# Kernel optimization log

Measured on AMD Instinct MI355X. Metric: run time of the kernel, lower is better.

The kernel has to match this reference:

```python
import jax, jax.numpy as jnp
import numpy as np

N_ATOMS = 10000
N_EDGES = 160000
C_EMB = 32          # embedding_size
N_RBF = 32          # radial_features
Z_MAX = 119
CUTOFF = 5.0


def setup_inputs() -> dict:
    key = jax.random.key(0)
    ks = jax.random.split(key, 8)
    atomic_numbers = jax.random.randint(ks[0], (N_ATOMS,), 0, Z_MAX)
    neighbour_index = jax.random.randint(ks[1], (2, N_EDGES), 0, N_ATOMS)
    edge_vectors = jax.random.normal(ks[2], (N_EDGES, 3), dtype=jnp.float32) * 2.0
    z_table = jax.random.normal(ks[3], (Z_MAX, C_EMB), dtype=jnp.float32) * 0.1
    z_map_W = jax.random.normal(ks[4], (C_EMB, 2 * C_EMB), dtype=jnp.float32) * 0.1
    dense_W = jax.random.normal(ks[5], (3 * C_EMB, N_RBF), dtype=jnp.float32) * 0.1
    dense_b = jax.random.normal(ks[6], (3 * C_EMB,), dtype=jnp.float32) * 0.1
    # PhysNet-style exponential RBF parameters (graph-pes ExponentialRBF)
    c_inf = float(np.exp(-CUTOFF))
    rbf_centres = jnp.linspace(c_inf, 1.0, N_RBF, dtype=jnp.float32)
    beta_val = (2.0 / N_RBF * (1.0 - c_inf)) ** -2
    rbf_beta = jnp.full((N_RBF,), beta_val, dtype=jnp.float32)
    return {
        'atomic_numbers': atomic_numbers,
        'neighbour_index': neighbour_index,
        'edge_vectors': edge_vectors,
        'z_table': z_table,
        'z_map_W': z_map_W,
        'dense_W': dense_W,
        'dense_b': dense_b,
        'rbf_beta': rbf_beta,
        'rbf_centres': rbf_centres,
    }


def reference(atomic_numbers, neighbour_index, edge_vectors, z_table,
              z_map_W, dense_W, dense_b, rbf_beta, rbf_centres):
    # --- geometry -----------------------------------------------------
    r = jnp.linalg.norm(edge_vectors, axis=-1)              # [E]
    r_hat = edge_vectors / r[:, None]                       # [E,3]
    vx, vy, vz = r_hat[:, 0], r_hat[:, 1], r_hat[:, 2]
    zero = jnp.zeros_like(vx)
    # skew-symmetric A_0 (matches torch stack ordering)
    A0 = jnp.stack([zero, -vz, vy,
                    vz, zero, -vx,
                    -vy, vx, zero], axis=1).reshape(-1, 3, 3)   # [E,3,3]
    eye = jnp.eye(3, dtype=edge_vectors.dtype)
    outer = r_hat[:, :, None] * r_hat[:, None, :]            # [E,3,3]
    trace_mean = jnp.trace(outer, axis1=-2, axis2=-1) / 3.0  # [E]
    S0 = 0.5 * (outer + jnp.swapaxes(outer, -1, -2)) - trace_mean[:, None, None] * eye
    # --- species embedding ---------------------------------------------
    h_atom = z_table[atomic_numbers]                         # [N,C]
    h_i = h_atom[neighbour_index[0]]                         # [E,C]
    h_j = h_atom[neighbour_index[1]]                         # [E,C]
    h_z = jnp.concatenate([h_i, h_j], axis=-1) @ z_map_W.T   # [E,C]
    # --- radial embedding (exp RBF -> Linear, x cosine envelope) -------
    rbf = jnp.exp(-rbf_beta[None, :] *
                  (jnp.exp(-r)[:, None] - rbf_centres[None, :]) ** 2)  # [E,R]
    h_r = rbf @ dense_W.T + dense_b                          # [E,3C]
    env = jnp.where(r < CUTOFF,
                    0.5 * (jnp.cos(jnp.pi * r / CUTOFF) + 1.0), 0.0)
    h_r = h_r * env[:, None]
    # --- combine --------------------------------------------------------
    c = h_r * jnp.tile(h_z, (1, 3))                          # [E,3C]
    C = h_z.shape[-1]
    c_I, c_A, c_S = c[:, :C], c[:, C:2 * C], c[:, 2 * C:]
    X_I = c_I[:, :, None, None] * eye                        # [E,C,3,3]
    X_A = c_A[:, :, None, None] * A0[:, None, :, :]          # [E,C,3,3]
    X_S = c_S[:, :, None, None] * S0[:, None, :, :]          # [E,C,3,3]
    return X_I, X_A, X_S
```

## Files before the change

### kernel.cpp

```cpp
#include <hip/hip_runtime.h>

#define N_EDGES 160000
#define C_EMB 32
#define N_RBF 32
#define Z_MAX 119

typedef float floatx4 __attribute__((ext_vector_type(4)));

#define PI_F 3.14159265358979323f
#define RSZ ((size_t)N_EDGES * 288)

__global__ __launch_bounds__(256) void k0_tables(
    const float* __restrict__ zt,
    const float* __restrict__ zw,
    float* __restrict__ FG)
{
    int i = blockIdx.x * 256 + threadIdx.x;
    if (i >= 2 * Z_MAX * C_EMB) return;
    int which = i / (Z_MAX * C_EMB);
    int j = i - which * Z_MAX * C_EMB;
    int z = j >> 5, cc = j & 31;
    const float* wrow = zw + cc * 64 + which * 32;
    const float* zrow = zt + z * 32;
    float acc = 0.0f;
    #pragma unroll
    for (int k = 0; k < 32; ++k) acc += zrow[k] * wrow[k];
    FG[i] = acc;
}

#define EPA 64
#define TA 256

__global__ __launch_bounds__(TA) void kA_features(
    const int* __restrict__ atomic_numbers,
    const int* __restrict__ nbr,
    const float* __restrict__ ev,
    const float* __restrict__ dense_W,
    const float* __restrict__ dense_b,
    const float* __restrict__ rbf_beta,
    const float* __restrict__ rbf_centres,
    const float* __restrict__ FG,
    float* __restrict__ rec)
{
    __shared__ int   s_zi[EPA];
    __shared__ int   s_zj[EPA];
    __shared__ float s_rbf[EPA][N_RBF];
    __shared__ float s_env[EPA];

    const int tid = threadIdx.x;
    const int e0 = blockIdx.x * EPA;

    if (tid < EPA)            s_zi[tid]       = atomic_numbers[nbr[e0 + tid]];
    else if (tid < 2 * EPA)   s_zj[tid - EPA] = atomic_numbers[nbr[N_EDGES + e0 + tid - EPA]];

    for (int idx = tid; idx < EPA * N_RBF; idx += TA) {
        int e = idx >> 5, n = idx & 31, ge = e0 + e;
        float x = ev[ge * 3 + 0], y = ev[ge * 3 + 1], z = ev[ge * 3 + 2];
        float r = sqrtf(x * x + y * y + z * z);
        float d = __expf(-r) - rbf_centres[n];
        s_rbf[e][n] = __expf(-rbf_beta[n] * d * d);
        if (n == 0)
            s_env[e] = (r < 5.0f) ? 0.5f * (__cosf(PI_F * r * 0.2f) + 1.0f) : 0.0f;
    }

    for (int idx = tid; idx < EPA * 27; idx += TA) {
        int e = idx / 27, t = idx - e * 27, ge = e0 + e;
        float x = ev[ge * 3 + 0], y = ev[ge * 3 + 1], z = ev[ge * 3 + 2];
        float rinv = rsqrtf(x * x + y * y + z * z);
        float vx = x * rinv, vy = y * rinv, vz = z * rinv;
        float val;
        if (t < 9) {
            val = (t == 0 || t == 4 || t == 8) ? 1.0f : 0.0f;
        } else if (t < 18) {
            int p = t - 9;
            switch (p) {
                case 1: val = -vz; break;
                case 2: val =  vy; break;
                case 3: val =  vz; break;
                case 5: val = -vx; break;
                case 6: val = -vy; break;
                case 7: val =  vx; break;
                default: val = 0.0f; break;
            }
        } else {
            int p = t - 18;
            int i = p / 3, j = p - 3 * i;
            float ri = (i == 0) ? vx : ((i == 1) ? vy : vz);
            float rj = (j == 0) ? vx : ((j == 1) ? vy : vz);
            val = ri * rj - ((i == j) ? (1.0f / 3.0f) : 0.0f);
        }
        rec[(size_t)ge * 128 + 96 + t] = val;
    }
    __syncthreads();

    const float* Ft = FG;
    const float* Gt = FG + Z_MAX * C_EMB;
    for (int idx = tid; idx < EPA * 96; idx += TA) {
        int e = idx / 96, m = idx - e * 96, ge = e0 + e;
        int cc = m & 31;
        const float4* Wd  = (const float4*)(dense_W + m * 32);
        const float4* rb4 = (const float4*)s_rbf[e];
        float acc = dense_b[m];
        #pragma unroll
        for (int n = 0; n < 8; ++n) {
            float4 w = Wd[n]; float4 rv = rb4[n];
            acc += w.x * rv.x + w.y * rv.y + w.z * rv.z + w.w * rv.w;
        }
        float hz = Ft[s_zi[e] * 32 + cc] + Gt[s_zj[e] * 32 + cc];
        rec[(size_t)ge * 128 + m] = acc * s_env[e] * hz;
    }
}

#define BBLK 1024
#define BT 256
#define NPAIR (N_EDGES / 2)

__global__ __launch_bounds__(BT) void kB_expand(
    const float* __restrict__ rec,
    float* __restrict__ out)
{
    __shared__ float lds[BT / 64][256];

    const int tid  = threadIdx.x;
    const int lane = tid & 63;
    const int w    = tid >> 6;
    const int gw   = blockIdx.x * (BT / 64) + w;
    const int NW   = BBLK * (BT / 64);

    int el[3], ccc[3][4], ppp[3][4];
    #pragma unroll
    for (int s = 0; s < 3; ++s) {
        int q = s * 64 + lane;
        int e_l = q / 72;
        int qq = q - 72 * e_l;
        el[s] = (q < 144) ? e_l : 0;
        #pragma unroll
        for (int u = 0; u < 4; ++u) {
            int f = 4 * qq + u;
            ccc[s][u] = f / 9;
            ppp[s][u] = f - 9 * (f / 9);
        }
    }

    float* sc = lds[w];
    const floatx4* rec4 = (const floatx4*)rec;
    const int half = lane >> 5, sub = lane & 31;

    floatx4 g = rec4[(size_t)(2 * gw + half) * 32 + sub];

    for (int p = gw; p < NPAIR; p += NW) {
        ((floatx4*)sc)[half * 32 + sub] = g;

        int pn = p + NW;
        floatx4 gn = g;
        if (pn < NPAIR) gn = rec4[(size_t)(2 * pn + half) * 32 + sub];

        #pragma unroll
        for (int r = 0; r < 3; ++r) {
            float* ob = out + (size_t)r * RSZ + (size_t)(2 * p) * 288;
            #pragma unroll
            for (int s = 0; s < 2; ++s) {
                floatx4 v;
                #pragma unroll
                for (int u = 0; u < 4; ++u) {
                    v[u] = sc[el[s] * 128 + 32 * r + ccc[s][u]]
                         * sc[el[s] * 128 + 96 + 9 * r + ppp[s][u]];
                }
                ((floatx4*)ob)[s * 64 + lane] = v;
            }
            if (lane < 16) {
                floatx4 v;
                #pragma unroll
                for (int u = 0; u < 4; ++u) {
                    v[u] = sc[el[2] * 128 + 32 * r + ccc[2][u]]
                         * sc[el[2] * 128 + 96 + 9 * r + ppp[2][u]];
                }
                ((floatx4*)ob)[128 + lane] = v;
            }
        }
        g = gn;
    }
}

#define EPBF 16
#define TF 256

__global__ __launch_bounds__(TF) void edge_embed_fallback(
    const int* __restrict__ atomic_numbers,
    const int* __restrict__ nbr,
    const float* __restrict__ ev,
    const float* __restrict__ z_table,
    const float* __restrict__ z_map_W,
    const float* __restrict__ dense_W,
    const float* __restrict__ dense_b,
    const float* __restrict__ rbf_beta,
    const float* __restrict__ rbf_centres,
    float* __restrict__ out)
{
    __shared__ float s_hi[EPBF][C_EMB];
    __shared__ float s_hj[EPBF][C_EMB];
    __shared__ float s_rbf[EPBF][N_RBF];
    __shared__ float s_hz[EPBF][C_EMB];
    __shared__ float s_c[EPBF][96];
    __shared__ float s_basis[EPBF][28];

    const int tid = threadIdx.x;
    const int e0 = blockIdx.x * EPBF;

    for (int idx = tid; idx < EPBF * C_EMB; idx += TF) {
        int e = idx >> 5, k = idx & 31, ge = e0 + e;
        s_hi[e][k] = z_table[atomic_numbers[nbr[ge]] * C_EMB + k];
        s_hj[e][k] = z_table[atomic_numbers[nbr[N_EDGES + ge]] * C_EMB + k];
    }
    for (int idx = tid; idx < EPBF * N_RBF; idx += TF) {
        int e = idx >> 5, n = idx & 31, ge = e0 + e;
        float x = ev[ge * 3 + 0], y = ev[ge * 3 + 1], z = ev[ge * 3 + 2];
        float r = sqrtf(x * x + y * y + z * z);
        float d = __expf(-r) - rbf_centres[n];
        s_rbf[e][n] = __expf(-rbf_beta[n] * d * d);
        if (n == 0)
            s_basis[e][27] = (r < 5.0f) ? 0.5f * (__cosf(PI_F * r * 0.2f) + 1.0f) : 0.0f;
    }
    for (int idx = tid; idx < EPBF * 27; idx += TF) {
        int e = idx / 27, t = idx - e * 27, ge = e0 + e;
        float x = ev[ge * 3 + 0], y = ev[ge * 3 + 1], z = ev[ge * 3 + 2];
        float rinv = rsqrtf(x * x + y * y + z * z);
        float vx = x * rinv, vy = y * rinv, vz = z * rinv;
        float val;
        if (t < 9) val = (t == 0 || t == 4 || t == 8) ? 1.0f : 0.0f;
        else if (t < 18) {
            int p = t - 9;
            switch (p) {
                case 1: val = -vz; break;
                case 2: val =  vy; break;
                case 3: val =  vz; break;
                case 5: val = -vx; break;
                case 6: val = -vy; break;
                case 7: val =  vx; break;
                default: val = 0.0f; break;
            }
        } else {
            int p = t - 18;
            int i = p / 3, j = p - 3 * i;
            float ri = (i == 0) ? vx : ((i == 1) ? vy : vz);
            float rj = (j == 0) ? vx : ((j == 1) ? vy : vz);
            val = ri * rj - ((i == j) ? (1.0f / 3.0f) : 0.0f);
        }
        s_basis[e][t] = val;
    }
    __syncthreads();
    for (int idx = tid; idx < EPBF * C_EMB; idx += TF) {
        int e = idx >> 5, cc = idx & 31;
        const float4* Wi  = (const float4*)(z_map_W + cc * 64);
        const float4* hi4 = (const float4*)s_hi[e];
        const float4* hj4 = (const float4*)s_hj[e];
        float acc = 0.0f;
        #pragma unroll
        for (int k = 0; k < 8; ++k) {
            float4 w = Wi[k]; float4 h = hi4[k];
            acc += w.x * h.x + w.y * h.y + w.z * h.z + w.w * h.w;
        }
        #pragma unroll
        for (int k = 0; k < 8; ++k) {
            float4 w = Wi[8 + k]; float4 h = hj4[k];
            acc += w.x * h.x + w.y * h.y + w.z * h.z + w.w * h.w;
        }
        s_hz[e][cc] = acc;
    }
    __syncthreads();
    for (int idx = tid; idx < EPBF * 96; idx += TF) {
        int e = idx / 96, m = idx - e * 96;
        int cc = m & 31;
        const float4* Wd  = (const float4*)(dense_W + m * 32);
        const float4* rb4 = (const float4*)s_rbf[e];
        float acc = dense_b[m];
        #pragma unroll
        for (int n = 0; n < 8; ++n) {
            float4 w = Wd[n]; float4 rv = rb4[n];
            acc += w.x * rv.x + w.y * rv.y + w.z * rv.z + w.w * rv.w;
        }
        s_c[e][m] = acc * s_basis[e][27] * s_hz[e][cc];
    }
    __syncthreads();
    float* outI = out + (size_t)e0 * 288;
    float* outA = out + RSZ + (size_t)e0 * 288;
    float* outS = out + 2 * RSZ + (size_t)e0 * 288;
    const int NQ = EPBF * 288 / 4;
    for (int q = tid; q < NQ; q += TF) {
        int fbase = q * 4;
        floatx4 aI, aA, aS;
        #pragma unroll
        for (int u = 0; u < 4; ++u) {
            int f = fbase + u;
            int e = f / 288;
            int rem = f - e * 288;
            int cc = rem / 9;
            int p = rem - cc * 9;
            aI[u] = s_c[e][cc]      * s_basis[e][p];
            aA[u] = s_c[e][32 + cc] * s_basis[e][9 + p];
            aS[u] = s_c[e][64 + cc] * s_basis[e][18 + p];
        }
        ((floatx4*)outI)[q] = aI;
        ((floatx4*)outA)[q] = aA;
        ((floatx4*)outS)[q] = aS;
    }
}

extern "C" void kernel_launch(void* const* d_in, const int* in_sizes, int n_in,
                              void* d_out, int out_size, void* d_ws, size_t ws_size,
                              hipStream_t stream) {
    const int*   an  = (const int*)d_in[0];
    const int*   nbr = (const int*)d_in[1];
    const float* ev  = (const float*)d_in[2];
    const float* zt  = (const float*)d_in[3];
    const float* zw  = (const float*)d_in[4];
    const float* dw  = (const float*)d_in[5];
    const float* db  = (const float*)d_in[6];
    const float* rb  = (const float*)d_in[7];
    const float* rc  = (const float*)d_in[8];
    float* outp = (float*)d_out;

    const size_t rec_f = (size_t)N_EDGES * 128;
    const size_t fg_f  = 2 * Z_MAX * C_EMB;
    const size_t need  = (rec_f + fg_f) * sizeof(float);

    if (ws_size >= need) {
        float* rec = (float*)d_ws;
        float* FG  = rec + rec_f;
        k0_tables<<<dim3((2 * Z_MAX * C_EMB + 255) / 256), 256, 0, stream>>>(zt, zw, FG);
        kA_features<<<dim3(N_EDGES / EPA), TA, 0, stream>>>(
            an, nbr, ev, dw, db, rb, rc, FG, rec);
        kB_expand<<<dim3(BBLK), BT, 0, stream>>>(rec, outp);
    } else {
        edge_embed_fallback<<<dim3(N_EDGES / EPBF), TF, 0, stream>>>(
            an, nbr, ev, zt, zw, dw, db, rb, rc, outp);
    }
}
```

Baseline: 378.0 us.

## Expand one edge per wavefront with direct global loads instead of LDS staging

The expand kernel now gives each wavefront one edge per iteration instead of a pair staged through shared memory. Each lane reads its coefficient and basis values straight from the per-edge record, which should hit in cache, and picks between two adjacent channel values with a select. It drops the LDS round trip and the software prefetch, and doubles the grid to 2048 blocks. The trade-off is more scalar global loads per lane and more underused lanes on the 72-vector tail (only 8 of 64 lanes active).

Result: slower. 468.9 us (+24.1%).

```diff
diff --git a/kernel.cpp b/kernel.cpp
--- a/kernel.cpp
+++ b/kernel.cpp
@@ -111,74 +111,76 @@
     }
 }
 
-#define BBLK 1024
-#define BT 256
-#define NPAIR (N_EDGES / 2)
-
-__global__ __launch_bounds__(BT) void kB_expand(
+#define TB 256
+#define NB 2048
+
+__global__ __launch_bounds__(TB) void kB_expand(
     const float* __restrict__ rec,
     float* __restrict__ out)
 {
-    __shared__ float lds[BT / 64][256];
-
-    const int tid  = threadIdx.x;
-    const int lane = tid & 63;
-    const int w    = tid >> 6;
-    const int gw   = blockIdx.x * (BT / 64) + w;
-    const int NW   = BBLK * (BT / 64);
-
-    int el[3], ccc[3][4], ppp[3][4];
+    const int lane = threadIdx.x & 63;
+    const int gw   = (blockIdx.x * TB + threadIdx.x) >> 6;
+    const int NW   = NB * (TB >> 6);
+
+    int cbase[2];
+    int sel[2][4];
+    int pp[2][4];
     #pragma unroll
-    for (int s = 0; s < 3; ++s) {
+    for (int s = 0; s < 2; ++s) {
         int q = s * 64 + lane;
-        int e_l = q / 72;
-        int qq = q - 72 * e_l;
-        el[s] = (q < 144) ? e_l : 0;
+        if (q >= 72) q = 71;
+        int f0 = 4 * q;
+        cbase[s] = f0 / 9;
         #pragma unroll
         for (int u = 0; u < 4; ++u) {
-            int f = 4 * qq + u;
-            ccc[s][u] = f / 9;
-            ppp[s][u] = f - 9 * (f / 9);
-        }
-    }
-
-    float* sc = lds[w];
-    const floatx4* rec4 = (const floatx4*)rec;
-    const int half = lane >> 5, sub = lane & 31;
-
-    floatx4 g = rec4[(size_t)(2 * gw + half) * 32 + sub];
-
-    for (int p = gw; p < NPAIR; p += NW) {
-        ((floatx4*)sc)[half * 32 + sub] = g;
-
-        int pn = p + NW;
-        floatx4 gn = g;
-        if (pn < NPAIR) gn = rec4[(size_t)(2 * pn + half) * 32 + sub];
-
+            int f = f0 + u;
+            int c = f / 9;
+            sel[s][u] = c - cbase[s];
+            pp[s][u]  = f - 9 * c;
+        }
+    }
+    const bool t1 = (lane < 8);
+
+    for (int e = gw; e < N_EDGES; e += NW) {
+        const float* row = rec + (size_t)e * 128;
+
+        float c0a[3], c0b[3], b0[3][4];
         #pragma unroll
         for (int r = 0; r < 3; ++r) {
-            float* ob = out + (size_t)r * RSZ + (size_t)(2 * p) * 288;
+            c0a[r] = row[32 * r + cbase[0]];
+            c0b[r] = row[32 * r + cbase[0] + 1];
             #pragma unroll
-            for (int s = 0; s < 2; ++s) {
-                floatx4 v;
+            for (int u = 0; u < 4; ++u)
+                b0[r][u] = row[96 + 9 * r + pp[0][u]];
+        }
+        float c1a[3], c1b[3], b1[3][4];
+        if (t1) {
+            #pragma unroll
+            for (int r = 0; r < 3; ++r) {
+                c1a[r] = row[32 * r + cbase[1]];
+                c1b[r] = row[32 * r + cbase[1] + 1];
                 #pragma unroll
-                for (int u = 0; u < 4; ++u) {
-                    v[u] = sc[el[s] * 128 + 32 * r + ccc[s][u]]
-                         * sc[el[s] * 128 + 96 + 9 * r + ppp[s][u]];
-                }
-                ((floatx4*)ob)[s * 64 + lane] = v;
+                for (int u = 0; u < 4; ++u)
+                    b1[r][u] = row[96 + 9 * r + pp[1][u]];
             }
-            if (lane < 16) {
-                floatx4 v;
+        }
+
+        #pragma unroll
+        for (int r = 0; r < 3; ++r) {
+            float* ob = out + (size_t)r * RSZ + (size_t)e * 288;
+            floatx4 v;
+            #pragma unroll
+            for (int u = 0; u < 4; ++u)
+                v[u] = (sel[0][u] ? c0b[r] : c0a[r]) * b0[r][u];
+            *(floatx4*)(ob + 4 * lane) = v;
+            if (t1) {
+                floatx4 w;
                 #pragma unroll
-                for (int u = 0; u < 4; ++u) {
-                    v[u] = sc[el[2] * 128 + 32 * r + ccc[2][u]]
-                         * sc[el[2] * 128 + 96 + 9 * r + ppp[2][u]];
-                }
-                ((floatx4*)ob)[128 + lane] = v;
+                for (int u = 0; u < 4; ++u)
+                    w[u] = (sel[1][u] ? c1b[r] : c1a[r]) * b1[r][u];
+                *(floatx4*)(ob + 256 + 4 * lane) = w;
             }
         }
-        g = gn;
     }
 }
 
@@ -330,7 +332,7 @@
         k0_tables<<<dim3((2 * Z_MAX * C_EMB + 255) / 256), 256, 0, stream>>>(zt, zw, FG);
         kA_features<<<dim3(N_EDGES / EPA), TA, 0, stream>>>(
             an, nbr, ev, dw, db, rb, rc, FG, rec);
-        kB_expand<<<dim3(BBLK), BT, 0, stream>>>(rec, outp);
+        kB_expand<<<dim3(NB), TB, 0, stream>>>(rec, outp);
     } else {
         edge_embed_fallback<<<dim3(N_EDGES / EPBF), TF, 0, stream>>>(
             an, nbr, ev, zt, zw, dw, db, rb, rc, outp);
```

## Replace persistent wave expand kernel with per-block streaming kernel and hoist geometry

Applied to the files above, without the earlier changes.

The output-expansion kernel goes from a persistent grid, where each wave loops over edge pairs with a register prefetch, to a non-persistent grid of 10000 blocks. Each block stages 16 edges of the compact record into shared memory and writes all three output tensors with float4 stores. The features kernel now computes r, exp(-r), the envelope and the unit vector once per edge into shared memory, so the RBF and tensor loops no longer recompute them. The trade-offs are more block launches, the loss of cross-iteration prefetch, and per-element index divisions in the store loop.

Result: faster. 360.9 us (-4.5%).

```diff
diff --git a/kernel.cpp b/kernel.cpp
--- a/kernel.cpp
+++ b/kernel.cpp
@@ -18,7 +18,7 @@
     int i = blockIdx.x * 256 + threadIdx.x;
     if (i >= 2 * Z_MAX * C_EMB) return;
     int which = i / (Z_MAX * C_EMB);
-    int j = i - which * Z_MAX * C_EMB;
+    int j = i - which * (Z_MAX * C_EMB);
     int z = j >> 5, cc = j & 31;
     const float* wrow = zw + cc * 64 + which * 32;
     const float* zrow = zt + z * 32;
@@ -42,32 +42,38 @@
     const float* __restrict__ FG,
     float* __restrict__ rec)
 {
-    __shared__ int   s_zi[EPA];
-    __shared__ int   s_zj[EPA];
+    __shared__ float s_er[EPA], s_env[EPA];
+    __shared__ float s_vx[EPA], s_vy[EPA], s_vz[EPA];
+    __shared__ int   s_zi[EPA], s_zj[EPA];
     __shared__ float s_rbf[EPA][N_RBF];
-    __shared__ float s_env[EPA];
 
     const int tid = threadIdx.x;
     const int e0 = blockIdx.x * EPA;
 
-    if (tid < EPA)            s_zi[tid]       = atomic_numbers[nbr[e0 + tid]];
-    else if (tid < 2 * EPA)   s_zj[tid - EPA] = atomic_numbers[nbr[N_EDGES + e0 + tid - EPA]];
+    if (tid < EPA) {
+        int ge = e0 + tid;
+        float x = ev[ge * 3 + 0], y = ev[ge * 3 + 1], z = ev[ge * 3 + 2];
+        float r2 = x * x + y * y + z * z;
+        float r = sqrtf(r2);
+        float rinv = rsqrtf(r2);
+        s_er[tid]  = __expf(-r);
+        s_env[tid] = (r < 5.0f) ? 0.5f * (__cosf(PI_F * r * 0.2f) + 1.0f) : 0.0f;
+        s_vx[tid] = x * rinv; s_vy[tid] = y * rinv; s_vz[tid] = z * rinv;
+    } else if (tid < 2 * EPA) {
+        s_zi[tid - EPA] = atomic_numbers[nbr[e0 + tid - EPA]];
+    } else if (tid < 3 * EPA) {
+        s_zj[tid - 2 * EPA] = atomic_numbers[nbr[N_EDGES + e0 + tid - 2 * EPA]];
+    }
+    __syncthreads();
 
     for (int idx = tid; idx < EPA * N_RBF; idx += TA) {
-        int e = idx >> 5, n = idx & 31, ge = e0 + e;
-        float x = ev[ge * 3 + 0], y = ev[ge * 3 + 1], z = ev[ge * 3 + 2];
-        float r = sqrtf(x * x + y * y + z * z);
-        float d = __expf(-r) - rbf_centres[n];
+        int e = idx >> 5, n = idx & 31;
+        float d = s_er[e] - rbf_centres[n];
         s_rbf[e][n] = __expf(-rbf_beta[n] * d * d);
-        if (n == 0)
-            s_env[e] = (r < 5.0f) ? 0.5f * (__cosf(PI_F * r * 0.2f) + 1.0f) : 0.0f;
-    }
-
+    }
     for (int idx = tid; idx < EPA * 27; idx += TA) {
         int e = idx / 27, t = idx - e * 27, ge = e0 + e;
-        float x = ev[ge * 3 + 0], y = ev[ge * 3 + 1], z = ev[ge * 3 + 2];
-        float rinv = rsqrtf(x * x + y * y + z * z);
-        float vx = x * rinv, vy = y * rinv, vz = z * rinv;
+        float vx = s_vx[e], vy = s_vy[e], vz = s_vz[e];
         float val;
         if (t < 9) {
             val = (t == 0 || t == 4 || t == 8) ? 1.0f : 0.0f;
@@ -111,74 +117,41 @@
     }
 }
 
-#define BBLK 1024
-#define BT 256
-#define NPAIR (N_EDGES / 2)
-
-__global__ __launch_bounds__(BT) void kB_expand(
+#define KEPB 16
+#define TB 256
+
+__global__ __launch_bounds__(TB) void kB_stream(
     const float* __restrict__ rec,
     float* __restrict__ out)
 {
-    __shared__ float lds[BT / 64][256];
-
-    const int tid  = threadIdx.x;
-    const int lane = tid & 63;
-    const int w    = tid >> 6;
-    const int gw   = blockIdx.x * (BT / 64) + w;
-    const int NW   = BBLK * (BT / 64);
-
-    int el[3], ccc[3][4], ppp[3][4];
+    __shared__ float s[KEPB * 128];
+
+    const int tid = threadIdx.x;
+    const int e0 = blockIdx.x * KEPB;
+
+    const floatx4* r4 = (const floatx4*)(rec + (size_t)e0 * 128);
+    ((floatx4*)s)[tid]       = r4[tid];
+    ((floatx4*)s)[tid + 256] = r4[tid + 256];
+    __syncthreads();
+
     #pragma unroll
-    for (int s = 0; s < 3; ++s) {
-        int q = s * 64 + lane;
-        int e_l = q / 72;
-        int qq = q - 72 * e_l;
-        el[s] = (q < 144) ? e_l : 0;
-        #pragma unroll
-        for (int u = 0; u < 4; ++u) {
-            int f = 4 * qq + u;
-            ccc[s][u] = f / 9;
-            ppp[s][u] = f - 9 * (f / 9);
-        }
-    }
-
-    float* sc = lds[w];
-    const floatx4* rec4 = (const floatx4*)rec;
-    const int half = lane >> 5, sub = lane & 31;
-
-    floatx4 g = rec4[(size_t)(2 * gw + half) * 32 + sub];
-
-    for (int p = gw; p < NPAIR; p += NW) {
-        ((floatx4*)sc)[half * 32 + sub] = g;
-
-        int pn = p + NW;
-        floatx4 gn = g;
-        if (pn < NPAIR) gn = rec4[(size_t)(2 * pn + half) * 32 + sub];
-
-        #pragma unroll
-        for (int r = 0; r < 3; ++r) {
-            float* ob = out + (size_t)r * RSZ + (size_t)(2 * p) * 288;
+    for (int r = 0; r < 3; ++r) {
+        float* ob = out + (size_t)r * RSZ + (size_t)e0 * 288;
+        for (int q = tid; q < KEPB * 288 / 4; q += TB) {
+            int f = 4 * q;
+            int e = f / 288;
+            int rem = f - e * 288;
+            int cc = rem / 9;
+            int p = rem - cc * 9;
+            const float* se = s + e * 128;
+            floatx4 v;
             #pragma unroll
-            for (int s = 0; s < 2; ++s) {
-                floatx4 v;
-                #pragma unroll
-                for (int u = 0; u < 4; ++u) {
-                    v[u] = sc[el[s] * 128 + 32 * r + ccc[s][u]]
-                         * sc[el[s] * 128 + 96 + 9 * r + ppp[s][u]];
-                }
-                ((floatx4*)ob)[s * 64 + lane] = v;
+            for (int u = 0; u < 4; ++u) {
+                int cross = (p + u >= 9);
+                v[u] = se[32 * r + cc + cross] * se[96 + 9 * r + p + u - 9 * cross];
             }
-            if (lane < 16) {
-                floatx4 v;
-                #pragma unroll
-                for (int u = 0; u < 4; ++u) {
-                    v[u] = sc[el[2] * 128 + 32 * r + ccc[2][u]]
-                         * sc[el[2] * 128 + 96 + 9 * r + ppp[2][u]];
-                }
-                ((floatx4*)ob)[128 + lane] = v;
-            }
-        }
-        g = gn;
+            *(floatx4*)(ob + f) = v;
+        }
     }
 }
 
@@ -330,7 +303,7 @@
         k0_tables<<<dim3((2 * Z_MAX * C_EMB + 255) / 256), 256, 0, stream>>>(zt, zw, FG);
         kA_features<<<dim3(N_EDGES / EPA), TA, 0, stream>>>(
             an, nbr, ev, dw, db, rb, rc, FG, rec);
-        kB_expand<<<dim3(BBLK), BT, 0, stream>>>(rec, outp);
+        kB_stream<<<dim3(N_EDGES / KEPB), TB, 0, stream>>>(rec, outp);
     } else {
         edge_embed_fallback<<<dim3(N_EDGES / EPBF), TF, 0, stream>>>(
             an, nbr, ev, zt, zw, dw, db, rb, rc, outp);
```
